# Performance work log

Measured on AMD Instinct MI355X. Metric: run time of the kernel, lower is better.

The kernel has to match this reference:

```python
import jax, jax.numpy as jnp
import numpy as np

B, F, D_IN, H, HEADS, NC = 2048, 64, 32, 128, 4, 16
EPG = 128            # random intra-graph edges per graph
N = B * F            # 131072 nodes
E = B * EPG          # 262144 edges (self-loops added in reference, like PyG GATConv)
LRELU_ATT = 0.2      # PyG GATConv negative_slope
LRELU_CLS = 0.01     # nn.LeakyReLU default


def setup_inputs() -> dict:
    key = jax.random.key(0)
    ks = jax.random.split(key, 24)
    emb = jax.random.normal(ks[0], (B, F, D_IN), jnp.float32)
    # per-graph random connectivity, offset so graphs are disjoint
    src_l = jax.random.randint(ks[1], (B, EPG), 0, F)
    tgt_l = jax.random.randint(ks[2], (B, EPG), 0, F)
    off = (jnp.arange(B) * F)[:, None]
    edge_index = jnp.stack([(src_l + off).reshape(-1), (tgt_l + off).reshape(-1)]).astype(jnp.int32)
    batch_idx = jnp.repeat(jnp.arange(B), F).astype(jnp.int32)
    s = 0.05
    return {
        'emb': emb, 'edge_index': edge_index, 'batch_idx': batch_idx,
        # fused aligner (single unique dim 32)
        'W_align': s * jax.random.normal(ks[3], (D_IN, H), jnp.float32),
        'b_align': jnp.zeros((H,), jnp.float32),
        'gate_logits': jnp.full((F,), 2.2, jnp.float32),
        # GATConv 1: in=H, out=H per head, heads=4, concat
        'W1': s * jax.random.normal(ks[4], (H, HEADS * H), jnp.float32),
        'a_src1': s * jax.random.normal(ks[5], (HEADS, H), jnp.float32),
        'a_dst1': s * jax.random.normal(ks[6], (HEADS, H), jnp.float32),
        'b1': jnp.zeros((HEADS * H,), jnp.float32),
        # GATConv 2: in=HEADS*H, out=H, heads=1, concat=False
        'W2': s * jax.random.normal(ks[7], (HEADS * H, H), jnp.float32),
        'a_src2': s * jax.random.normal(ks[8], (1, H), jnp.float32),
        'a_dst2': s * jax.random.normal(ks[9], (1, H), jnp.float32),
        'b2': jnp.zeros((H,), jnp.float32),
        # classifier MLP
        'Wc1': s * jax.random.normal(ks[10], (H, H // 2), jnp.float32),
        'bc1': jnp.zeros((H // 2,), jnp.float32),
        'Wc2': s * jax.random.normal(ks[11], (H // 2, NC), jnp.float32),
        'bc2': jnp.zeros((NC,), jnp.float32),
    }


def gat_layer(x, src, tgt, W, a_src, a_dst, b, concat):
    heads, dout = a_src.shape
    n = x.shape[0]
    h = (x @ W).reshape(n, heads, dout)                       # [N,h,d]
    e = jax.nn.leaky_relu(jnp.einsum('nhd,hd->nh', h, a_src)[src]
                          + jnp.einsum('nhd,hd->nh', h, a_dst)[tgt], LRELU_ATT)  # [E,h]
    m = jax.ops.segment_max(e, tgt, num_segments=n)           # segment softmax over in-neighbors
    p = jnp.exp(e - m[tgt])
    ssum = jax.ops.segment_sum(p, tgt, num_segments=n)
    alpha = p / (ssum[tgt] + 1e-16)
    out = jax.ops.segment_sum(h[src] * alpha[:, :, None], tgt, num_segments=n)
    out = out.reshape(n, heads * dout) if concat else out.mean(axis=1)
    return out + b


def reference(emb, edge_index, batch_idx, W_align, b_align, gate_logits,
              W1, a_src1, a_dst1, b1, W2, a_src2, a_dst2, b2, Wc1, bc1, Wc2, bc2):
    n = emb.shape[0] * emb.shape[1]
    aligned = emb @ W_align + b_align                         # fused align: [B,F,H]
    gate = jax.nn.sigmoid(gate_logits)                        # [F]
    x = (aligned * gate[None, :, None]).reshape(n, -1)        # gated node features [N,H]
    # add self-loops (GATConv default), eval mode -> dropout is identity
    loops = jnp.arange(n, dtype=edge_index.dtype)
    src = jnp.concatenate([edge_index[0], loops])
    tgt = jnp.concatenate([edge_index[1], loops])
    x = gat_layer(x, src, tgt, W1, a_src1, a_dst1, b1, True)  # [N, 4*H]
    x = jax.nn.elu(x)
    x = gat_layer(x, src, tgt, W2, a_src2, a_dst2, b2, False) # [N, H]
    gsum = jax.ops.segment_sum(x, batch_idx, num_segments=B)  # global_mean_pool
    cnt = jax.ops.segment_sum(jnp.ones((n, 1), x.dtype), batch_idx, num_segments=B)
    g = gsum / cnt                                            # [B, H]
    hc = jax.nn.leaky_relu(g @ Wc1 + bc1, LRELU_CLS)
    logits = hc @ Wc2 + bc2                                   # [B, NC]
    return logits, gate
```

## Files before the change

### kernel.cpp

```cpp
#include <hip/hip_runtime.h>
#include <math.h>

#define BLK 256

constexpr int Bg    = 2048;
constexpr int Fn    = 64;
constexpr int DIN   = 32;
constexpr int Hd    = 128;
constexpr int HEADS = 4;
constexpr int NC    = 16;
constexpr int EPG   = 128;
constexpr int Etot  = Bg * EPG;
constexpr int W1C   = HEADS * Hd;
constexpr int NSTR  = 68;
constexpr int EROW  = 136;
constexpr int PROW  = 68;
constexpr int NE    = EPG + Fn;

typedef __attribute__((ext_vector_type(8))) __bf16 bf16x8;
typedef __attribute__((ext_vector_type(4))) __bf16 bf16x4;
typedef __attribute__((ext_vector_type(4))) float  f32x4;

__device__ __align__(16) __bf16 g_wcombT[W1C * DIN];
__device__ float g_c1[W1C];
__device__ float g_c1s[16];
__device__ __align__(16) __bf16 g_w1F[HEADS*8*64*8];
__device__ __align__(16) __bf16 g_w2F[HEADS*4*8*64*8];
__device__ __align__(16) __bf16 g_wscF[HEADS*4*64*8];
__device__ __align__(16) __bf16 g_bs1F[64*8];

__global__ __launch_bounds__(BLK) void prep1(
    const float* __restrict__ Wa, const float* __restrict__ ba,
    const float* __restrict__ W1)
{
  __shared__ float WaS[DIN * Hd];
  const int tid = threadIdx.x;
  for (int i = tid; i < DIN * Hd; i += BLK) {
    int k = i >> 7, m = i & 127;
    WaS[m * DIN + k] = Wa[i];
  }
  __syncthreads();

  int i = blockIdx.x * BLK + tid;
  if (i < DIN * W1C) {
    int k = i & 31, n = i >> 5;
    float a0 = 0.f, a1 = 0.f, a2 = 0.f, a3 = 0.f;
    #pragma unroll
    for (int m = 0; m < Hd; m += 4) {
      a0 += WaS[(m  )*DIN + k] * W1[(m  )*W1C + n];
      a1 += WaS[(m+1)*DIN + k] * W1[(m+1)*W1C + n];
      a2 += WaS[(m+2)*DIN + k] * W1[(m+2)*W1C + n];
      a3 += WaS[(m+3)*DIN + k] * W1[(m+3)*W1C + n];
    }
    g_wcombT[i] = (__bf16)(a0 + a1 + a2 + a3);
  } else if (i < DIN*W1C + W1C) {
    int n = i - DIN*W1C;
    float a0 = 0.f, a1 = 0.f, a2 = 0.f, a3 = 0.f;
    #pragma unroll
    for (int m = 0; m < Hd; m += 4) {
      a0 += ba[m  ] * W1[(m  )*W1C + n];
      a1 += ba[m+1] * W1[(m+1)*W1C + n];
      a2 += ba[m+2] * W1[(m+2)*W1C + n];
      a3 += ba[m+3] * W1[(m+3)*W1C + n];
    }
    g_c1[n] = a0 + a1 + a2 + a3;
  }
}

constexpr int R_W2F  = 65536;
constexpr int R_W1F  = 16384;
constexpr int R_WSCZ = 8192;
constexpr int R_WSCD = 4096;
constexpr int R_BS1Z = 512;
constexpr int R_BS1D = 1024;
constexpr int R_C1S  = 128;
constexpr int B0 = R_W2F;
constexpr int B1 = B0 + R_W1F;
constexpr int B2 = B1 + R_WSCZ;
constexpr int B3 = B2 + R_WSCD;
constexpr int B4 = B3 + R_BS1Z;
constexpr int B5 = B4 + R_BS1D;
constexpr int P2_TOT = B5 + R_C1S;

__global__ __launch_bounds__(BLK) void prep2(
    const float* __restrict__ W2,
    const float* __restrict__ as1, const float* __restrict__ ad1,
    const float* __restrict__ as2, const float* __restrict__ ad2)
{
  int i = blockIdx.x * BLK + threadIdx.x;
  if (i < B0) {
    int k = i >> 7, n = i & 127;
    int hh = k >> 7, Ks = (k >> 5) & 3, q = (k >> 3) & 3, j = k & 7;
    int Nt = n >> 4, l = n & 15;
    int idx = (((hh*4 + Ks)*8 + Nt)*64 + (q*16 + l))*8 + j;
    g_w2F[idx] = (__bf16)W2[i];
  } else if (i < B1) {
    int j = i - B0;
    int jj = j & 7, lane = (j >> 3) & 63, T = j >> 9;
    int hh = T >> 3, Nt = T & 7;
    int q = lane >> 4, l = lane & 15;
    g_w1F[j] = g_wcombT[(hh*Hd + Nt*16 + l)*DIN + q*8 + jj];
  } else if (i < B2) {
    int j = i - B1;
    int lane = (j >> 3) & 63, c = lane & 15;
    if (c >= 2) g_wscF[j] = (__bf16)0.f;
  } else if (i < B3) {
    int j = i - B2;
    int p = j & 3, c = (j >> 2) & 1, k = j >> 3;
    const float* av = c ? ad2 : as2;
    float a0 = 0.f, a1 = 0.f, a2 = 0.f, a3 = 0.f;
    #pragma unroll
    for (int q = 0; q < 32; q += 4) {
      int f = p*32 + q;
      a0 += W2[(size_t)k*Hd + f    ] * av[f    ];
      a1 += W2[(size_t)k*Hd + f + 1] * av[f + 1];
      a2 += W2[(size_t)k*Hd + f + 2] * av[f + 2];
      a3 += W2[(size_t)k*Hd + f + 3] * av[f + 3];
    }
    float a = a0 + a1 + a2 + a3;
    a += __shfl_xor(a, 1);
    a += __shfl_xor(a, 2);
    if (p == 0) {
      int T = k >> 5, q2 = (k >> 3) & 3, jj = k & 7;
      g_wscF[(T*64 + q2*16 + c)*8 + jj] = (__bf16)a;
    }
  } else if (i < B4) {
    int j = i - B3;
    int lane = j >> 3, c = lane & 15;
    if (c >= 8) g_bs1F[j] = (__bf16)0.f;
  } else if (i < B5) {
    int j = i - B4;
    int p = j & 3, c = (j >> 2) & 7, kk = j >> 5;
    int h = c >> 1;
    const float* av = (c & 1) ? (ad1 + h*Hd) : (as1 + h*Hd);
    float a0 = 0.f, a1 = 0.f, a2 = 0.f, a3 = 0.f;
    #pragma unroll
    for (int q = 0; q < 32; q += 4) {
      int f = p*32 + q;
      a0 += (float)g_wcombT[(h*Hd + f    )*DIN + kk] * av[f    ];
      a1 += (float)g_wcombT[(h*Hd + f + 1)*DIN + kk] * av[f + 1];
      a2 += (float)g_wcombT[(h*Hd + f + 2)*DIN + kk] * av[f + 2];
      a3 += (float)g_wcombT[(h*Hd + f + 3)*DIN + kk] * av[f + 3];
    }
    float a = a0 + a1 + a2 + a3;
    a += __shfl_xor(a, 1);
    a += __shfl_xor(a, 2);
    if (p == 0) {
      int q2 = kk >> 3, jj = kk & 7;
      g_bs1F[(q2*16 + c)*8 + jj] = (__bf16)a;
    }
  } else if (i < P2_TOT) {
    int j = i - B5;
    int p = j & 7, c = j >> 3;
    float a = 0.f;
    if (c < 8) {
      int h = c >> 1;
      const float* av = (c & 1) ? (ad1 + h*Hd) : (as1 + h*Hd);
      #pragma unroll
      for (int q = 0; q < 16; ++q) {
        int f = p*16 + q;
        a += g_c1[h*Hd + f] * av[f];
      }
    }
    a += __shfl_xor(a, 1);
    a += __shfl_xor(a, 2);
    a += __shfl_xor(a, 4);
    if (p == 0) g_c1s[c] = a;
  }
}

__global__ __launch_bounds__(BLK, 3) void gat_main(
    const float* __restrict__ emb, const int* __restrict__ ei,
    const float* __restrict__ gate_logits,
    const float* __restrict__ b1, const float* __restrict__ b2,
    const float* __restrict__ Wc1, const float* __restrict__ bc1,
    const float* __restrict__ Wc2, const float* __restrict__ bc2,
    float* __restrict__ out)
{
  __shared__ __align__(16) __bf16 hT[Hd * NSTR];
  __shared__ __align__(16) __bf16 eluS[Fn * EROW];
  __shared__ __align__(16) __bf16 Pbf[Fn * PROW];
  __shared__ float sS1s[HEADS][Fn], sS1d[HEADS][Fn];
  __shared__ float sSrc[Fn], sDst[Fn], sSum[Fn], gateS[Fn];
  __shared__ float gpool[Hd], hcS[Fn];
  __shared__ __align__(16) __bf16 wS[Fn];

  unsigned* cells = (unsigned*)eluS;

  const int b    = blockIdx.x;
  const int tid  = threadIdx.x;
  const int lane = tid & 63;
  const int wv   = tid >> 6;
  const int quad = lane >> 4;
  const int l15  = lane & 15;
  const int nodeBase = wv * 16;
  const int m0   = wv * 32;
  const int base = b * Fn;

  const f32x4 zero4 = {0.f, 0.f, 0.f, 0.f};

  int es = 0, et = 0, ecell = 0;
  if (tid < NE) {
    if (tid < EPG) {
      es = ei[(size_t)b*EPG + tid] - base;
      et = ei[(size_t)Etot + (size_t)b*EPG + tid] - base;
    } else {
      es = et = tid - EPG;
    }
    ecell = et * Fn + es;
  }
  #pragma unroll
  for (int i = 0; i < 16; ++i) cells[tid + i*BLK] = 0u;
  {
    float4* p4 = (float4*)Pbf;
    const float4 z4 = {0.f,0.f,0.f,0.f};
    p4[tid] = z4; p4[tid + 256] = z4;
    if (tid < 32) p4[tid + 512] = z4;
  }
  if (tid < Fn) {
    float g = 1.f / (1.f + expf(-gate_logits[tid]));
    gateS[tid] = g; sSum[tid] = 0.f;
    if (b == 0) out[Bg*NC + tid] = g;
  }
  bf16x8 Af;
  {
    const float* ar = emb + ((size_t)base + nodeBase + l15) * DIN + quad * 8;
    float4 e0 = *(const float4*)ar;
    float4 e1 = *(const float4*)(ar + 4);
    Af[0]=(__bf16)e0.x; Af[1]=(__bf16)e0.y; Af[2]=(__bf16)e0.z; Af[3]=(__bf16)e0.w;
    Af[4]=(__bf16)e1.x; Af[5]=(__bf16)e1.y; Af[6]=(__bf16)e1.z; Af[7]=(__bf16)e1.w;
  }
  __syncthreads();

  bool rep = false;
  if (tid < NE) rep = (atomicAdd(&cells[ecell], 1u) == 0u);
  {
    bf16x8 Bs = *(const bf16x8*)(g_bs1F + lane*8);
    f32x4 ds = __builtin_amdgcn_mfma_f32_16x16x32_bf16(Af, Bs, zero4, 0, 0, 0);
    if (l15 < 8) {
      const float cc = g_c1s[l15];
      const int h = l15 >> 1;
      float* dstArr = (l15 & 1) ? &sS1d[h][0] : &sS1s[h][0];
      #pragma unroll
      for (int r = 0; r < 4; ++r) {
        int m = nodeBase + quad*4 + r;
        dstArr[m] = gateS[m] * (ds[r] + cc);
      }
    }
  }
  __syncthreads();

  float fm = 0.f;
  if (tid < NE && rep) fm = (float)cells[ecell];

  float gq[4];
  #pragma unroll
  for (int r = 0; r < 4; ++r) gq[r] = gateS[nodeBase + quad*4 + r];

  f32x4 acc[8];
  #pragma unroll
  for (int i = 0; i < 8; ++i) acc[i] = zero4;
  f32x4 accS = zero4;

  for (int hh = 0; hh < HEADS; ++hh) {
    #pragma unroll
    for (int Nt = 0; Nt < 8; ++Nt) {
      const int n = Nt*16 + l15;
      bf16x8 Bf = *(const bf16x8*)(g_w1F + ((hh*8 + Nt)*64 + lane)*8);
      f32x4 d = __builtin_amdgcn_mfma_f32_16x16x32_bf16(Af, Bf, zero4, 0, 0, 0);
      const float c1v = g_c1[hh*Hd + n];
      bf16x4 hw;
      #pragma unroll
      for (int r = 0; r < 4; ++r) hw[r] = (__bf16)((d[r] + c1v) * gq[r]);
      *(bf16x4*)(hT + n*NSTR + nodeBase + quad*4) = hw;
    }
    if (tid < NE && rep) {
      float e = sS1s[hh][es] + sS1d[hh][et];
      e = (e > 0.f) ? e : 0.2f * e;
      float pe = fm * __expf(e);
      Pbf[et*PROW + es] = (__bf16)pe;
      atomicAdd(&sSum[et], pe);
    }
    __syncthreads();

    {
      bf16x8 Ac[2][2];
      #pragma unroll
      for (int Mi = 0; Mi < 2; ++Mi)
        #pragma unroll
        for (int Ks = 0; Ks < 2; ++Ks)
          Ac[Mi][Ks] = *(const bf16x8*)(hT + (m0 + Mi*16 + l15)*NSTR + Ks*32 + quad*8);
      float4 b1v[2];
      #pragma unroll
      for (int Mi = 0; Mi < 2; ++Mi)
        b1v[Mi] = *(const float4*)&b1[hh*Hd + m0 + Mi*16 + quad*4];
      #pragma unroll
      for (int Nt = 0; Nt < 4; ++Nt) {
        bf16x8 B0f = *(const bf16x8*)(Pbf + (Nt*16 + l15)*PROW + quad*8);
        bf16x8 B1f = *(const bf16x8*)(Pbf + (Nt*16 + l15)*PROW + 32 + quad*8);
        const int t = Nt*16 + l15;
        const float si = 1.f / (sSum[t] + 1e-16f);
        #pragma unroll
        for (int Mi = 0; Mi < 2; ++Mi) {
          f32x4 d = __builtin_amdgcn_mfma_f32_16x16x32_bf16(Ac[Mi][0], B0f, zero4, 0, 0, 0);
          d = __builtin_amdgcn_mfma_f32_16x16x32_bf16(Ac[Mi][1], B1f, d, 0, 0, 0);
          bf16x4 w;
          #pragma unroll
          for (int r = 0; r < 4; ++r) {
            float hv = d[r]*si + b1v[Mi][r];
            hv = (hv > 0.f) ? hv : (__expf(hv) - 1.f);
            w[r] = (__bf16)hv;
          }
          *(bf16x4*)(eluS + t*EROW + m0 + Mi*16 + quad*4) = w;
        }
      }
    }
    __syncthreads();

    #pragma unroll
    for (int Ks = 0; Ks < 4; ++Ks) {
      bf16x8 A2 = *(const bf16x8*)(eluS + (nodeBase + l15)*EROW + Ks*32 + quad*8);
      #pragma unroll
      for (int Nt = 0; Nt < 8; ++Nt) {
        bf16x8 B2 = *(const bf16x8*)(g_w2F + (((hh*4 + Ks)*8 + Nt)*64 + lane)*8);
        acc[Nt] = __builtin_amdgcn_mfma_f32_16x16x32_bf16(A2, B2, acc[Nt], 0, 0, 0);
      }
      bf16x8 Bs2 = *(const bf16x8*)(g_wscF + ((hh*4 + Ks)*64 + lane)*8);
      accS = __builtin_amdgcn_mfma_f32_16x16x32_bf16(A2, Bs2, accS, 0, 0, 0);
    }
    {
      float4* p4 = (float4*)Pbf;
      const float4 z4 = {0.f,0.f,0.f,0.f};
      p4[tid] = z4; p4[tid + 256] = z4;
      if (tid < 32) p4[tid + 512] = z4;
      if (tid < Fn) sSum[tid] = 0.f;
    }
    __syncthreads();
  }

  #pragma unroll
  for (int Nt = 0; Nt < 8; ++Nt) {
    const int n = Nt*16 + l15;
    bf16x4 hw;
    #pragma unroll
    for (int r = 0; r < 4; ++r) hw[r] = (__bf16)acc[Nt][r];
    *(bf16x4*)(hT + n*NSTR + nodeBase + quad*4) = hw;
  }
  if (l15 == 0) {
    #pragma unroll
    for (int r = 0; r < 4; ++r) sSrc[nodeBase + quad*4 + r] = accS[r];
  } else if (l15 == 1) {
    #pragma unroll
    for (int r = 0; r < 4; ++r) sDst[nodeBase + quad*4 + r] = accS[r];
  }
  __syncthreads();

  if (tid < NE && rep) {
    float e = sSrc[es] + sDst[et];
    e = (e > 0.f) ? e : 0.2f * e;
    float pe = fm * __expf(e);
    Pbf[et*PROW + es] = (__bf16)pe;
    atomicAdd(&sSum[et], pe);
  }
  __syncthreads();

  {
    const int s_ = tid >> 2, part = tid & 3;
    float a = 0.f;
    #pragma unroll
    for (int q = 0; q < 16; ++q) {
      const int t = part*16 + q;
      a += (1.f / (sSum[t] + 1e-16f)) * (float)Pbf[t*PROW + s_];
    }
    a += __shfl_xor(a, 1);
    a += __shfl_xor(a, 2);
    if (part == 0) wS[s_] = (__bf16)(a * (1.f/64.f));
  }
  __syncthreads();

  {
    #pragma unroll
    for (int Mi = 0; Mi < 2; ++Mi) {
      f32x4 d = zero4;
      #pragma unroll
      for (int Ks = 0; Ks < 2; ++Ks) {
        bf16x8 A = *(const bf16x8*)(hT + (m0 + Mi*16 + l15)*NSTR + Ks*32 + quad*8);
        bf16x8 Bw = *(const bf16x8*)(wS + Ks*32 + quad*8);
        d = __builtin_amdgcn_mfma_f32_16x16x32_bf16(A, Bw, d, 0, 0, 0);
      }
      if (l15 == 0) {
        #pragma unroll
        for (int r = 0; r < 4; ++r) {
          const int f = m0 + Mi*16 + quad*4 + r;
          gpool[f] = d[r] + b2[f];
        }
      }
    }
  }
  __syncthreads();

  {
    const int c = tid >> 2, p = tid & 3;
    float a = 0.f;
    #pragma unroll
    for (int i = 0; i < 32; ++i) {
      const int k = p*32 + i;
      a += gpool[k] * Wc1[k*Fn + c];
    }
    a += __shfl_xor(a, 1);
    a += __shfl_xor(a, 2);
    if (p == 0) {
      a += bc1[c];
      hcS[c] = (a > 0.f) ? a : 0.01f * a;
    }
  }
  __syncthreads();

  {
    const int c = tid >> 4, p = tid & 15;
    float a = 0.f;
    #pragma unroll
    for (int i = 0; i < 4; ++i) {
      const int k = p*4 + i;
      a += hcS[k] * Wc2[k*NC + c];
    }
    a += __shfl_xor(a, 1);
    a += __shfl_xor(a, 2);
    a += __shfl_xor(a, 4);
    a += __shfl_xor(a, 8);
    if (p == 0) out[b*NC + c] = a + bc2[c];
  }
}

extern "C" void kernel_launch(void* const* d_in, const int* in_sizes, int n_in,
                              void* d_out, int out_size, void* d_ws, size_t ws_size,
                              hipStream_t stream) {
  const float* emb = (const float*)d_in[0];
  const int*   ei  = (const int*)  d_in[1];
  const float* Wa  = (const float*)d_in[3];
  const float* ba  = (const float*)d_in[4];
  const float* gl  = (const float*)d_in[5];
  const float* W1  = (const float*)d_in[6];
  const float* as1 = (const float*)d_in[7];
  const float* ad1 = (const float*)d_in[8];
  const float* b1  = (const float*)d_in[9];
  const float* W2  = (const float*)d_in[10];
  const float* as2 = (const float*)d_in[11];
  const float* ad2 = (const float*)d_in[12];
  const float* b2  = (const float*)d_in[13];
  const float* Wc1 = (const float*)d_in[14];
  const float* bc1 = (const float*)d_in[15];
  const float* Wc2 = (const float*)d_in[16];
  const float* bc2 = (const float*)d_in[17];
  float* out = (float*)d_out;

  const int prep1N = DIN*W1C + W1C;
  hipLaunchKernelGGL(prep1, dim3((prep1N + BLK - 1)/BLK), dim3(BLK), 0, stream,
                     Wa, ba, W1);
  hipLaunchKernelGGL(prep2, dim3((P2_TOT + BLK - 1)/BLK), dim3(BLK), 0, stream,
                     W2, as1, ad1, as2, ad2);
  hipLaunchKernelGGL(gat_main, dim3(Bg), dim3(BLK), 0, stream,
                     emb, ei, gl, b1, b2, Wc1, bc1, Wc2, bc2, out);
}
```

Before: 194.0 us.

## Precompute all head attention weights upfront and merge per-head barriers

Attention probabilities for all four heads are computed in one pass, each into its own shared-memory slot with its own sum array. The per-head loop then no longer needs its own edge-scoring phase and barrier. Each next head's feature projection is computed at the tail of the previous iteration, sharing that iteration's barrier. The node gate is folded into the bf16 input operand rather than applied after the matmul. Together these remove a barrier per head. The price is about 26 KB more shared memory per block, so launch bounds drop from 3 to 2 blocks per CU, and the gate fold changes rounding slightly.

```diff
diff --git a/kernel.cpp b/kernel.cpp
--- a/kernel.cpp
+++ b/kernel.cpp
@@ -169,7 +169,7 @@
   }
 }
 
-__global__ __launch_bounds__(BLK, 3) void gat_main(
+__global__ __launch_bounds__(BLK, 2) void gat_main(
     const float* __restrict__ emb, const int* __restrict__ ei,
     const float* __restrict__ gate_logits,
     const float* __restrict__ b1, const float* __restrict__ b2,
@@ -179,9 +179,10 @@
 {
   __shared__ __align__(16) __bf16 hT[Hd * NSTR];
   __shared__ __align__(16) __bf16 eluS[Fn * EROW];
-  __shared__ __align__(16) __bf16 Pbf[Fn * PROW];
+  __shared__ __align__(16) __bf16 Pbf[HEADS][Fn * PROW];
   __shared__ float sS1s[HEADS][Fn], sS1d[HEADS][Fn];
-  __shared__ float sSrc[Fn], sDst[Fn], sSum[Fn], gateS[Fn];
+  __shared__ float sSum[HEADS][Fn];
+  __shared__ float sSrc[Fn], sDst[Fn], gateS[Fn];
   __shared__ float gpool[Hd], hcS[Fn];
   __shared__ __align__(16) __bf16 wS[Fn];
 
@@ -212,28 +213,39 @@
   #pragma unroll
   for (int i = 0; i < 16; ++i) cells[tid + i*BLK] = 0u;
   {
-    float4* p4 = (float4*)Pbf;
+    float4* p4 = (float4*)&Pbf[0][0];
     const float4 z4 = {0.f,0.f,0.f,0.f};
-    p4[tid] = z4; p4[tid + 256] = z4;
-    if (tid < 32) p4[tid + 512] = z4;
-  }
+    #pragma unroll
+    for (int k = 0; k < 8; ++k) p4[tid + k*BLK] = z4;
+    if (tid < 128) p4[2048 + tid] = z4;
+  }
+  ((float*)sSum)[tid] = 0.f;
   if (tid < Fn) {
     float g = 1.f / (1.f + expf(-gate_logits[tid]));
-    gateS[tid] = g; sSum[tid] = 0.f;
+    gateS[tid] = g;
     if (b == 0) out[Bg*NC + tid] = g;
   }
-  bf16x8 Af;
+  float4 e0, e1;
   {
     const float* ar = emb + ((size_t)base + nodeBase + l15) * DIN + quad * 8;
-    float4 e0 = *(const float4*)ar;
-    float4 e1 = *(const float4*)(ar + 4);
-    Af[0]=(__bf16)e0.x; Af[1]=(__bf16)e0.y; Af[2]=(__bf16)e0.z; Af[3]=(__bf16)e0.w;
-    Af[4]=(__bf16)e1.x; Af[5]=(__bf16)e1.y; Af[6]=(__bf16)e1.z; Af[7]=(__bf16)e1.w;
+    e0 = *(const float4*)ar;
+    e1 = *(const float4*)(ar + 4);
   }
   __syncthreads();
 
   bool rep = false;
   if (tid < NE) rep = (atomicAdd(&cells[ecell], 1u) == 0u);
+
+  float gq[4];
+  #pragma unroll
+  for (int r = 0; r < 4; ++r) gq[r] = gateS[nodeBase + quad*4 + r];
+
+  bf16x8 Af;
+  {
+    const float gl = gateS[nodeBase + l15];
+    Af[0]=(__bf16)(e0.x*gl); Af[1]=(__bf16)(e0.y*gl); Af[2]=(__bf16)(e0.z*gl); Af[3]=(__bf16)(e0.w*gl);
+    Af[4]=(__bf16)(e1.x*gl); Af[5]=(__bf16)(e1.y*gl); Af[6]=(__bf16)(e1.z*gl); Af[7]=(__bf16)(e1.w*gl);
+  }
   {
     bf16x8 Bs = *(const bf16x8*)(g_bs1F + lane*8);
     f32x4 ds = __builtin_amdgcn_mfma_f32_16x16x32_bf16(Af, Bs, zero4, 0, 0, 0);
@@ -244,18 +256,36 @@
       #pragma unroll
       for (int r = 0; r < 4; ++r) {
         int m = nodeBase + quad*4 + r;
-        dstArr[m] = gateS[m] * (ds[r] + cc);
-      }
-    }
+        dstArr[m] = ds[r] + gq[r] * cc;
+      }
+    }
+  }
+  #pragma unroll
+  for (int Nt = 0; Nt < 8; ++Nt) {
+    const int n = Nt*16 + l15;
+    bf16x8 Bf = *(const bf16x8*)(g_w1F + ((0*8 + Nt)*64 + lane)*8);
+    f32x4 d = __builtin_amdgcn_mfma_f32_16x16x32_bf16(Af, Bf, zero4, 0, 0, 0);
+    const float c1v = g_c1[0*Hd + n];
+    bf16x4 hw;
+    #pragma unroll
+    for (int r = 0; r < 4; ++r) hw[r] = (__bf16)(d[r] + c1v * gq[r]);
+    *(bf16x4*)(hT + n*NSTR + nodeBase + quad*4) = hw;
   }
   __syncthreads();
 
   float fm = 0.f;
-  if (tid < NE && rep) fm = (float)cells[ecell];
-
-  float gq[4];
-  #pragma unroll
-  for (int r = 0; r < 4; ++r) gq[r] = gateS[nodeBase + quad*4 + r];
+  if (tid < NE && rep) {
+    fm = (float)cells[ecell];
+    #pragma unroll
+    for (int hh = 0; hh < HEADS; ++hh) {
+      float e = sS1s[hh][es] + sS1d[hh][et];
+      e = (e > 0.f) ? e : 0.2f * e;
+      float pe = fm * __expf(e);
+      Pbf[hh][et*PROW + es] = (__bf16)pe;
+      atomicAdd(&sSum[hh][et], pe);
+    }
+  }
+  __syncthreads();
 
   f32x4 acc[8];
   #pragma unroll
@@ -263,26 +293,6 @@
   f32x4 accS = zero4;
 
   for (int hh = 0; hh < HEADS; ++hh) {
-    #pragma unroll
-    for (int Nt = 0; Nt < 8; ++Nt) {
-      const int n = Nt*16 + l15;
-      bf16x8 Bf = *(const bf16x8*)(g_w1F + ((hh*8 + Nt)*64 + lane)*8);
-      f32x4 d = __builtin_amdgcn_mfma_f32_16x16x32_bf16(Af, Bf, zero4, 0, 0, 0);
-      const float c1v = g_c1[hh*Hd + n];
-      bf16x4 hw;
-      #pragma unroll
-      for (int r = 0; r < 4; ++r) hw[r] = (__bf16)((d[r] + c1v) * gq[r]);
-      *(bf16x4*)(hT + n*NSTR + nodeBase + quad*4) = hw;
-    }
-    if (tid < NE && rep) {
-      float e = sS1s[hh][es] + sS1d[hh][et];
-      e = (e > 0.f) ? e : 0.2f * e;
-      float pe = fm * __expf(e);
-      Pbf[et*PROW + es] = (__bf16)pe;
-      atomicAdd(&sSum[et], pe);
-    }
-    __syncthreads();
-
     {
       bf16x8 Ac[2][2];
       #pragma unroll
@@ -296,10 +306,10 @@
         b1v[Mi] = *(const float4*)&b1[hh*Hd + m0 + Mi*16 + quad*4];
       #pragma unroll
       for (int Nt = 0; Nt < 4; ++Nt) {
-        bf16x8 B0f = *(const bf16x8*)(Pbf + (Nt*16 + l15)*PROW + quad*8);
-        bf16x8 B1f = *(const bf16x8*)(Pbf + (Nt*16 + l15)*PROW + 32 + quad*8);
+        bf16x8 B0f = *(const bf16x8*)(Pbf[hh] + (Nt*16 + l15)*PROW + quad*8);
+        bf16x8 B1f = *(const bf16x8*)(Pbf[hh] + (Nt*16 + l15)*PROW + 32 + quad*8);
         const int t = Nt*16 + l15;
-        const float si = 1.f / (sSum[t] + 1e-16f);
+        const float si = 1.f / (sSum[hh][t] + 1e-16f);
         #pragma unroll
         for (int Mi = 0; Mi < 2; ++Mi) {
           f32x4 d = __builtin_amdgcn_mfma_f32_16x16x32_bf16(Ac[Mi][0], B0f, zero4, 0, 0, 0);
@@ -328,39 +338,51 @@
       bf16x8 Bs2 = *(const bf16x8*)(g_wscF + ((hh*4 + Ks)*64 + lane)*8);
       accS = __builtin_amdgcn_mfma_f32_16x16x32_bf16(A2, Bs2, accS, 0, 0, 0);
     }
-    {
-      float4* p4 = (float4*)Pbf;
+    if (hh == 0) {
+      float4* p4 = (float4*)&Pbf[0][0];
       const float4 z4 = {0.f,0.f,0.f,0.f};
       p4[tid] = z4; p4[tid + 256] = z4;
       if (tid < 32) p4[tid + 512] = z4;
-      if (tid < Fn) sSum[tid] = 0.f;
+      if (tid < Fn) sSum[0][tid] = 0.f;
+    }
+    if (hh < 3) {
+      #pragma unroll
+      for (int Nt = 0; Nt < 8; ++Nt) {
+        const int n = Nt*16 + l15;
+        bf16x8 Bf = *(const bf16x8*)(g_w1F + (((hh+1)*8 + Nt)*64 + lane)*8);
+        f32x4 d = __builtin_amdgcn_mfma_f32_16x16x32_bf16(Af, Bf, zero4, 0, 0, 0);
+        const float c1v = g_c1[(hh+1)*Hd + n];
+        bf16x4 hw;
+        #pragma unroll
+        for (int r = 0; r < 4; ++r) hw[r] = (__bf16)(d[r] + c1v * gq[r]);
+        *(bf16x4*)(hT + n*NSTR + nodeBase + quad*4) = hw;
+      }
+    } else {
+      #pragma unroll
+      for (int Nt = 0; Nt < 8; ++Nt) {
+        const int n = Nt*16 + l15;
+        bf16x4 hw;
+        #pragma unroll
+        for (int r = 0; r < 4; ++r) hw[r] = (__bf16)acc[Nt][r];
+        *(bf16x4*)(hT + n*NSTR + nodeBase + quad*4) = hw;
+      }
+      if (l15 == 0) {
+        #pragma unroll
+        for (int r = 0; r < 4; ++r) sSrc[nodeBase + quad*4 + r] = accS[r];
+      } else if (l15 == 1) {
+        #pragma unroll
+        for (int r = 0; r < 4; ++r) sDst[nodeBase + quad*4 + r] = accS[r];
+      }
     }
     __syncthreads();
   }
-
-  #pragma unroll
-  for (int Nt = 0; Nt < 8; ++Nt) {
-    const int n = Nt*16 + l15;
-    bf16x4 hw;
-    #pragma unroll
-    for (int r = 0; r < 4; ++r) hw[r] = (__bf16)acc[Nt][r];
-    *(bf16x4*)(hT + n*NSTR + nodeBase + quad*4) = hw;
-  }
-  if (l15 == 0) {
-    #pragma unroll
-    for (int r = 0; r < 4; ++r) sSrc[nodeBase + quad*4 + r] = accS[r];
-  } else if (l15 == 1) {
-    #pragma unroll
-    for (int r = 0; r < 4; ++r) sDst[nodeBase + quad*4 + r] = accS[r];
-  }
-  __syncthreads();
 
   if (tid < NE && rep) {
     float e = sSrc[es] + sDst[et];
     e = (e > 0.f) ? e : 0.2f * e;
     float pe = fm * __expf(e);
-    Pbf[et*PROW + es] = (__bf16)pe;
-    atomicAdd(&sSum[et], pe);
+    Pbf[0][et*PROW + es] = (__bf16)pe;
+    atomicAdd(&sSum[0][et], pe);
   }
   __syncthreads();
 
@@ -370,7 +392,7 @@
     #pragma unroll
     for (int q = 0; q < 16; ++q) {
       const int t = part*16 + q;
-      a += (1.f / (sSum[t] + 1e-16f)) * (float)Pbf[t*PROW + s_];
+      a += (1.f / (sSum[0][t] + 1e-16f)) * (float)Pbf[0][t*PROW + s_];
     }
     a += __shfl_xor(a, 1);
     a += __shfl_xor(a, 2);
```

After: 209.4 us. +7.9%, slower.
